# Optimization experiments

Measured on AMD Instinct MI355X. Metric: run time of the kernel, lower is better.

The kernel has to match this reference:

```python
import jax, jax.numpy as jnp
import numpy as np

BS, V, H, W = 2, 4, 24, 24
C, K, L, NH = 256, 16, 6, 8
DH = C // NH
FF = 4 * C
EPS = 1e-5


def _ln(x, w, b):
    m = jnp.mean(x, axis=-1, keepdims=True)
    v = jnp.mean((x - m) ** 2, axis=-1, keepdims=True)
    return (x - m) * jax.lax.rsqrt(v + EPS) * w + b


def _pe(x, W1, b1, W2, b2):
    # PositionEmbeddingLearnedMLP: Linear(3,C) -> ReLU -> Linear(C,C), channels-last
    return jax.nn.relu(x @ W1.T + b1) @ W2.T + b2


def setup_inputs():
    key = jax.random.key(0)
    ks = jax.random.split(key, 8)
    s = 0.02
    return {
        "feature": jax.random.normal(ks[0], (BS * V, C, H, W), jnp.float32),
        "xyz": jax.random.uniform(ks[1], (BS * V, H, W, 3), jnp.float32),
        "pe_W1": jax.random.normal(ks[2], (C, 3), jnp.float32) * s,
        "pe_b1": jnp.zeros((C,), jnp.float32),
        "pe_W2": jax.random.normal(ks[3], (C, C), jnp.float32) * s,
        "pe_b2": jnp.zeros((C,), jnp.float32),
        "Wqkv": jax.random.normal(ks[4], (L, 3 * C, C), jnp.float32) * s,
        "bqkv": jnp.zeros((L, 3 * C), jnp.float32),
        "Wo": jax.random.normal(ks[5], (L, C, C), jnp.float32) * s,
        "bo": jnp.zeros((L, C), jnp.float32),
        "ln_attn_w": jnp.ones((L, C), jnp.float32),
        "ln_attn_b": jnp.zeros((L, C), jnp.float32),
        "W1": jax.random.normal(ks[6], (L, FF, C), jnp.float32) * s,
        "b1": jnp.zeros((L, FF), jnp.float32),
        "W2": jax.random.normal(ks[7], (L, C, FF), jnp.float32) * s,
        "b2": jnp.zeros((L, C), jnp.float32),
        "ln_ffn_w": jnp.ones((L, C), jnp.float32),
        "ln_ffn_b": jnp.zeros((L, C), jnp.float32),
        "ln_out_w": jnp.ones((L, C), jnp.float32),
        "ln_out_b": jnp.zeros((L, C), jnp.float32),
    }


def _forward(feature, xyz, pe_W1, pe_b1, pe_W2, pe_b2, Wqkv, bqkv, Wo, bo,
             ln_attn_w, ln_attn_b, W1, b1, W2, b2, ln_ffn_w, ln_ffn_b,
             ln_out_w, ln_out_b):
    N = V * H * W
    # (B*V,C,H,W) -> (BS,N,C) ; (B*V,H,W,3) -> (BS,N,3) : flatten views+pixels
    feat = feature.reshape(BS, V, C, H, W).transpose(0, 1, 3, 4, 2).reshape(BS, N, C)
    pts = xyz.reshape(BS, N, 3)
    # per-batch KNN (self included), mirroring pointops.queryandgroup
    d2 = jnp.sum((pts[:, :, None, :] - pts[:, None, :, :]) ** 2, axis=-1)  # (BS,N,N)
    _, idx = jax.lax.top_k(-d2, K)  # (BS,N,K) nearest-neighbor indices
    grouped = jax.vmap(lambda p, i: p[i])(pts, idx)  # (BS,N,K,3)
    rel = grouped - pts[:, :, None, :]  # relative coords (use_xyz=True)
    q_pe = _pe(jnp.zeros((3,), feat.dtype), pe_W1, pe_b1, pe_W2, pe_b2)  # (C,)
    k_pe = _pe(rel, pe_W1, pe_b1, pe_W2, pe_b2).reshape(BS * N, K, C)
    idx_g = (idx + (jnp.arange(BS) * N)[:, None, None]).reshape(BS * N, K)
    out = feat.reshape(BS * N, C)
    for i in range(L):
        keyf = out[idx_g]  # (BN,K,C) per-layer neighbor gather
        # CrossAttentionLayer, pre-norm
        t2 = _ln(out, ln_attn_w[i], ln_attn_b[i])
        q = (t2 + q_pe) @ Wqkv[i, :C].T + bqkv[i, :C]
        k = (keyf + k_pe) @ Wqkv[i, C:2 * C].T + bqkv[i, C:2 * C]
        v = keyf @ Wqkv[i, 2 * C:].T + bqkv[i, 2 * C:]
        qh = q.reshape(-1, NH, DH)
        kh = k.reshape(-1, K, NH, DH)
        vh = v.reshape(-1, K, NH, DH)
        att = jax.nn.softmax(jnp.einsum('bhd,bkhd->bhk', qh, kh) * (DH ** -0.5), axis=-1)
        ao = jnp.einsum('bhk,bkhd->bhd', att, vh).reshape(-1, C) @ Wo[i].T + bo[i]
        out = out + ao
        # FFNLayer, pre-norm
        t2 = _ln(out, ln_ffn_w[i], ln_ffn_b[i])
        out = out + (jax.nn.relu(t2 @ W1[i].T + b1[i]) @ W2[i].T + b2[i])
        # extra per-layer LayerNorm
        out = _ln(out, ln_out_w[i], ln_out_b[i])
    return out.reshape(BS, V, H, W, C).transpose(0, 1, 4, 2, 3).reshape(BS * V, C, H, W)


def reference(feature, xyz, pe_W1, pe_b1, pe_W2, pe_b2, Wqkv, bqkv, Wo, bo,
              ln_attn_w, ln_attn_b, W1, b1, W2, b2, ln_ffn_w, ln_ffn_b,
              ln_out_w, ln_out_b):
    return _forward(feature, xyz, pe_W1, pe_b1, pe_W2, pe_b2, Wqkv, bqkv, Wo, bo,
                    ln_attn_w, ln_attn_b, W1, b1, W2, b2, ln_ffn_w, ln_ffn_b,
                    ln_out_w, ln_out_b)
```

## Files before the change

### kernel.cpp

```cpp
#include <hip/hip_runtime.h>
#include <math.h>

#define BS_ 2
#define V_ 4
#define H_ 24
#define W_ 24
#define N_ (V_*H_*W_)
#define BN_ (BS_*N_)
#define C_ 256
#define K_ 16
#define L_ 6
#define NH_ 8
#define DH_ 32
#define FF_ 1024

typedef __attribute__((ext_vector_type(4))) float f32x4;
typedef __attribute__((ext_vector_type(8))) short bf16x8;

__device__ inline unsigned short f2bf(float x) {
    unsigned u = __float_as_uint(x);
    unsigned r = u + 0x7fffu + ((u >> 16) & 1u);
    return (unsigned short)(r >> 16);
}
__device__ inline float bf2f(unsigned short h) {
    return __uint_as_float(((unsigned)h) << 16);
}

__global__ __launch_bounds__(256) void f2bf_kernel(const float* __restrict__ in,
                                                   unsigned short* __restrict__ out, int n) {
    int i = blockIdx.x*256 + threadIdx.x;
    if (i < n) out[i] = f2bf(in[i]);
}

__global__ __launch_bounds__(256) void reshape_in_kernel(const float* __restrict__ f,
                                                         float* __restrict__ outF,
                                                         unsigned short* __restrict__ outB) {
    int bn = blockIdx.x, c = threadIdx.x;
    int b = bn / N_, rem = bn % N_;
    int v = rem / (H_*W_), hw = rem % (H_*W_);
    float x = f[(((size_t)(b*V_ + v)*C_ + c)*(H_*W_)) + hw];
    outF[(size_t)bn*C_ + c] = x;
    outB[(size_t)bn*C_ + c] = f2bf(x);
}

__global__ __launch_bounds__(256) void reshape_out_kernel(const float* __restrict__ in,
                                                          float* __restrict__ o) {
    int bn = blockIdx.x, c = threadIdx.x;
    int b = bn / N_, rem = bn % N_;
    int v = rem / (H_*W_), hw = rem % (H_*W_);
    o[(((size_t)(b*V_ + v)*C_ + c)*(H_*W_)) + hw] = in[(size_t)bn*C_ + c];
}

__global__ __launch_bounds__(256) void knn_kernel(const float* __restrict__ pts,
                                                  int* __restrict__ idx) {
    int wid = threadIdx.x >> 6, lane = threadIdx.x & 63;
    int point = blockIdx.x*4 + wid;
    int b = point / N_;
    int il = point % N_;
    __shared__ float ps[N_*3];
    for (int l = threadIdx.x; l < N_*3; l += 256) ps[l] = pts[(size_t)b*N_*3 + l];
    __syncthreads();
    float qx = ps[il*3], qy = ps[il*3+1], qz = ps[il*3+2];
    unsigned long long key[36];
    #pragma unroll
    for (int s = 0; s < 36; ++s) {
        int j = lane + 64*s;
        float dx = qx - ps[j*3], dy = qy - ps[j*3+1], dz = qz - ps[j*3+2];
        float d2 = dx*dx + dy*dy + dz*dz;
        key[s] = ((unsigned long long)__float_as_uint(d2) << 32) | (unsigned)j;
    }
    for (int it = 0; it < K_; ++it) {
        unsigned long long best = key[0];
        #pragma unroll
        for (int s = 1; s < 36; ++s) best = key[s] < best ? key[s] : best;
        #pragma unroll
        for (int off = 32; off; off >>= 1) {
            unsigned long long o = __shfl_xor(best, off, 64);
            if (o < best) best = o;
        }
        int wj = (int)(best & 0xffffffffu);
        if (lane == 0) idx[point*K_ + it] = b*N_ + wj;
        if ((wj & 63) == lane) {
            int sw = wj >> 6;
            #pragma unroll
            for (int s = 0; s < 36; ++s) if (s == sw) key[s] = ~0ull;
        }
    }
}

__global__ __launch_bounds__(256) void qpe_kernel(const float* __restrict__ b1,
                                                  const float* __restrict__ W2,
                                                  const float* __restrict__ b2,
                                                  float* __restrict__ qpe) {
    __shared__ float h[C_];
    int tid = threadIdx.x;
    h[tid] = fmaxf(b1[tid], 0.f);
    __syncthreads();
    float acc = 0.f;
    for (int j = 0; j < C_; ++j) acc += h[j] * W2[(size_t)tid*C_ + j];
    qpe[tid] = acc + b2[tid];
}

__global__ __launch_bounds__(256) void pe_hidden_kernel(const float* __restrict__ pts,
                                                        const int* __restrict__ idx,
                                                        const float* __restrict__ W1,
                                                        const float* __restrict__ b1,
                                                        unsigned short* __restrict__ hidden) {
    int point = blockIdx.x;
    int c = threadIdx.x;
    __shared__ float rel[K_][3];
    if (threadIdx.x < K_*3) {
        int k = threadIdx.x / 3, ax = threadIdx.x % 3;
        int j = idx[point*K_ + k];
        rel[k][ax] = pts[(size_t)j*3 + ax] - pts[(size_t)point*3 + ax];
    }
    __syncthreads();
    float w0 = W1[c*3], w1 = W1[c*3+1], w2 = W1[c*3+2], bb = b1[c];
    #pragma unroll
    for (int k = 0; k < K_; ++k) {
        float v = rel[k][0]*w0 + rel[k][1]*w1 + rel[k][2]*w2 + bb;
        hidden[((size_t)point*K_ + k)*C_ + c] = f2bf(fmaxf(v, 0.f));
    }
}

template<int ACT, bool RES, int OMODE>
__global__ __launch_bounds__(256) void gemm_bf16(const unsigned short* __restrict__ A,
                                                 const unsigned short* __restrict__ W,
                                                 const float* __restrict__ bias,
                                                 const float* __restrict__ res,
                                                 float* __restrict__ outF,
                                                 unsigned short* __restrict__ outB,
                                                 int M, int P, int K) {
    const int BK = 32;
    __shared__ unsigned short As[64][BK+8];
    __shared__ unsigned short Ws[64][BK+8];
    int tid = threadIdx.x;
    int wave = tid >> 6, lane = tid & 63;
    int wr = wave >> 1, wc = wave & 1;
    int m0 = blockIdx.y * 64, n0 = blockIdx.x * 64;
    f32x4 acc[2][2];
    #pragma unroll
    for (int i = 0; i < 2; ++i)
        #pragma unroll
        for (int j = 0; j < 2; ++j) acc[i][j] = (f32x4){0.f, 0.f, 0.f, 0.f};

    int r = tid >> 2, ch = tid & 3;
    for (int k0 = 0; k0 < K; k0 += BK) {
        *(bf16x8*)&As[r][ch*8] = *(const bf16x8*)&A[(size_t)(m0 + r)*K + k0 + ch*8];
        *(bf16x8*)&Ws[r][ch*8] = *(const bf16x8*)&W[(size_t)(n0 + r)*K + k0 + ch*8];
        __syncthreads();
        int kf = (lane >> 4) * 8;
        bf16x8 af[2], wf[2];
        #pragma unroll
        for (int i = 0; i < 2; ++i) af[i] = *(const bf16x8*)&As[wr*32 + i*16 + (lane & 15)][kf];
        #pragma unroll
        for (int j = 0; j < 2; ++j) wf[j] = *(const bf16x8*)&Ws[wc*32 + j*16 + (lane & 15)][kf];
        #pragma unroll
        for (int i = 0; i < 2; ++i)
            #pragma unroll
            for (int j = 0; j < 2; ++j)
                acc[i][j] = __builtin_amdgcn_mfma_f32_16x16x32_bf16(af[i], wf[j], acc[i][j], 0, 0, 0);
        __syncthreads();
    }
    #pragma unroll
    for (int i = 0; i < 2; ++i) {
        #pragma unroll
        for (int j = 0; j < 2; ++j) {
            #pragma unroll
            for (int rg = 0; rg < 4; ++rg) {
                int m = m0 + wr*32 + i*16 + (lane >> 4)*4 + rg;
                int p = n0 + wc*32 + j*16 + (lane & 15);
                float v = acc[i][j][rg] + bias[p];
                if (ACT == 1) v = fmaxf(v, 0.f);
                if (RES) v += res[(size_t)m*P + p];
                if (OMODE != 2) outF[(size_t)m*P + p] = v;
                if (OMODE != 0) outB[(size_t)m*P + p] = f2bf(v);
            }
        }
    }
}

__global__ __launch_bounds__(256) void r_kernel(const unsigned short* __restrict__ q,
                                                const unsigned short* __restrict__ Wk,
                                                unsigned short* __restrict__ r) {
    int p0 = blockIdx.x * 16;
    int h = blockIdx.y;
    int tid = threadIdx.x;
    __shared__ float qs[16][DH_];
    for (int l = tid; l < 16*DH_; l += 256) {
        int p = l >> 5, d = l & 31;
        qs[p][d] = bf2f(q[(size_t)(p0 + p)*C_ + h*DH_ + d]);
    }
    __syncthreads();
    float acc[16] = {};
    for (int d = 0; d < DH_; ++d) {
        float w = bf2f(Wk[(size_t)(h*DH_ + d)*C_ + tid]);
        #pragma unroll
        for (int p = 0; p < 16; ++p) acc[p] += qs[p][d] * w;
    }
    #pragma unroll
    for (int p = 0; p < 16; ++p)
        r[(size_t)(p0 + p)*(NH_*C_) + h*C_ + tid] = f2bf(acc[p]);
}

__global__ __launch_bounds__(256) void attn_kernel(const unsigned short* __restrict__ q,
                                                   const unsigned short* __restrict__ kv,
                                                   const unsigned short* __restrict__ kpe,
                                                   const unsigned short* __restrict__ r,
                                                   const int* __restrict__ idx,
                                                   unsigned short* __restrict__ ao) {
    int wid = threadIdx.x >> 6, lane = threadIdx.x & 63;
    int point = blockIdx.x*4 + wid;
    __shared__ __align__(16) unsigned short vs[4][K_][264];
    __shared__ __align__(16) float atts[4][NH_][K_];
    int row = lane & 15;
    int off8 = (lane >> 4) * 8;
    int idx_l = idx[point*K_ + row];

    #pragma unroll
    for (int t = 0; t < 8; ++t) {
        int vr = 2*t + (lane >> 5);
        int j = __shfl(idx_l, vr, 64);
        int cc = (lane & 31) * 8;
        *(bf16x8*)&vs[wid][vr][cc] = *(const bf16x8*)&kv[(size_t)j*512 + 256 + cc];
    }

    f32x4 acc = {0.f, 0.f, 0.f, 0.f};
    const bf16x8 zero8 = {0,0,0,0,0,0,0,0};
    #pragma unroll
    for (int s = 0; s < 8; ++s) {
        bf16x8 a = *(const bf16x8*)&kpe[((size_t)point*K_ + row)*C_ + s*32 + off8];
        bf16x8 b = zero8;
        if (row < 8) b = *(const bf16x8*)&r[(size_t)point*NH_*C_ + row*C_ + s*32 + off8];
        acc = __builtin_amdgcn_mfma_f32_16x16x32_bf16(a, b, acc, 0, 0, 0);
    }
    #pragma unroll
    for (int s = 0; s < 8; ++s) {
        bf16x8 a = *(const bf16x8*)&kv[(size_t)idx_l*512 + s*32 + off8];
        bf16x8 b = zero8;
        if (row == 8 + s) b = *(const bf16x8*)&q[(size_t)point*C_ + s*32 + off8];
        acc = __builtin_amdgcn_mfma_f32_16x16x32_bf16(a, b, acc, 0, 0, 0);
    }

    const float scale = 0.1767766952966369f;
    float sv[4], m = -1e30f;
    #pragma unroll
    for (int rg = 0; rg < 4; ++rg) {
        float o = __shfl_xor(acc[rg], 8, 64);
        sv[rg] = (acc[rg] + o) * scale;
        m = fmaxf(m, sv[rg]);
    }
    m = fmaxf(m, __shfl_xor(m, 16, 64));
    m = fmaxf(m, __shfl_xor(m, 32, 64));
    float sum = 0.f;
    #pragma unroll
    for (int rg = 0; rg < 4; ++rg) { sv[rg] = __expf(sv[rg] - m); sum += sv[rg]; }
    sum += __shfl_xor(sum, 16, 64);
    sum += __shfl_xor(sum, 32, 64);
    float inv = 1.f / sum;
    if (row < 8) {
        f32x4 av = { sv[0]*inv, sv[1]*inv, sv[2]*inv, sv[3]*inv };
        *(f32x4*)&atts[wid][row][(lane >> 4) * 4] = av;
    }

    int h = lane >> 3;
    float att_f[16];
    #pragma unroll
    for (int u = 0; u < 4; ++u) {
        f32x4 t4 = *(const f32x4*)&atts[wid][h][u*4];
        att_f[u*4+0] = t4[0]; att_f[u*4+1] = t4[1]; att_f[u*4+2] = t4[2]; att_f[u*4+3] = t4[3];
    }
    int cbase = lane * 4;
    float o0 = 0.f, o1 = 0.f, o2 = 0.f, o3 = 0.f;
    #pragma unroll
    for (int k = 0; k < K_; ++k) {
        unsigned long long vv = *(const unsigned long long*)&vs[wid][k][cbase];
        unsigned lo = (unsigned)vv, hi = (unsigned)(vv >> 32);
        float a = att_f[k];
        o0 += a * __uint_as_float(lo << 16);
        o1 += a * __uint_as_float(lo & 0xffff0000u);
        o2 += a * __uint_as_float(hi << 16);
        o3 += a * __uint_as_float(hi & 0xffff0000u);
    }
    unsigned p0 = (unsigned)f2bf(o0) | ((unsigned)f2bf(o1) << 16);
    unsigned p1 = (unsigned)f2bf(o2) | ((unsigned)f2bf(o3) << 16);
    unsigned out2[2] = { p0, p1 };
    *(unsigned long long*)&ao[(size_t)point*C_ + cbase] = *(const unsigned long long*)out2;
}

template<int OMODE>
__global__ __launch_bounds__(256) void ln_kernel(const float* __restrict__ in,
                                                 const float* __restrict__ w,
                                                 const float* __restrict__ b,
                                                 const float* __restrict__ addvec,
                                                 float* __restrict__ outF,
                                                 unsigned short* __restrict__ outB) {
    int row = blockIdx.x, tid = threadIdx.x;
    float x = in[(size_t)row*C_ + tid];
    __shared__ float red[4];
    float v = x;
    #pragma unroll
    for (int off = 32; off; off >>= 1) v += __shfl_xor(v, off, 64);
    if ((tid & 63) == 0) red[tid >> 6] = v;
    __syncthreads();
    float mean = (red[0]+red[1]+red[2]+red[3]) * (1.f/C_);
    __syncthreads();
    float dx = x - mean;
    v = dx*dx;
    #pragma unroll
    for (int off = 32; off; off >>= 1) v += __shfl_xor(v, off, 64);
    if ((tid & 63) == 0) red[tid >> 6] = v;
    __syncthreads();
    float var = (red[0]+red[1]+red[2]+red[3]) * (1.f/C_);
    float y = dx * rsqrtf(var + 1e-5f) * w[tid] + b[tid];
    if (addvec) y += addvec[tid];
    if (OMODE != 2) outF[(size_t)row*C_ + tid] = y;
    outB[(size_t)row*C_ + tid] = f2bf(y);
}

__global__ __launch_bounds__(256) void ln2_kernel(const float* __restrict__ in,
                                                  const float* __restrict__ w1, const float* __restrict__ b1v,
                                                  const float* __restrict__ w2, const float* __restrict__ b2v,
                                                  const float* __restrict__ qpe,
                                                  float* __restrict__ outF, unsigned short* __restrict__ outB,
                                                  unsigned short* __restrict__ outT2) {
    int row = blockIdx.x, tid = threadIdx.x;
    float x = in[(size_t)row*C_ + tid];
    __shared__ float red[4];
    float v = x;
    #pragma unroll
    for (int off = 32; off; off >>= 1) v += __shfl_xor(v, off, 64);
    if ((tid & 63) == 0) red[tid >> 6] = v;
    __syncthreads();
    float mean = (red[0]+red[1]+red[2]+red[3]) * (1.f/C_);
    __syncthreads();
    float dx = x - mean;
    v = dx*dx;
    #pragma unroll
    for (int off = 32; off; off >>= 1) v += __shfl_xor(v, off, 64);
    if ((tid & 63) == 0) red[tid >> 6] = v;
    __syncthreads();
    float var = (red[0]+red[1]+red[2]+red[3]) * (1.f/C_);
    float y = dx * rsqrtf(var + 1e-5f) * w1[tid] + b1v[tid];
    outF[(size_t)row*C_ + tid] = y;
    outB[(size_t)row*C_ + tid] = f2bf(y);
    v = y;
    #pragma unroll
    for (int off = 32; off; off >>= 1) v += __shfl_xor(v, off, 64);
    __syncthreads();
    if ((tid & 63) == 0) red[tid >> 6] = v;
    __syncthreads();
    float mean2 = (red[0]+red[1]+red[2]+red[3]) * (1.f/C_);
    __syncthreads();
    float dy = y - mean2;
    v = dy*dy;
    #pragma unroll
    for (int off = 32; off; off >>= 1) v += __shfl_xor(v, off, 64);
    if ((tid & 63) == 0) red[tid >> 6] = v;
    __syncthreads();
    float var2 = (red[0]+red[1]+red[2]+red[3]) * (1.f/C_);
    float z = dy * rsqrtf(var2 + 1e-5f) * w2[tid] + b2v[tid] + qpe[tid];
    outT2[(size_t)row*C_ + tid] = f2bf(z);
}

extern "C" void kernel_launch(void* const* d_in, const int* in_sizes, int n_in,
                              void* d_out, int out_size, void* d_ws, size_t ws_size,
                              hipStream_t stream) {
    const float* feature  = (const float*)d_in[0];
    const float* xyz      = (const float*)d_in[1];
    const float* pe_W1    = (const float*)d_in[2];
    const float* pe_b1    = (const float*)d_in[3];
    const float* pe_W2    = (const float*)d_in[4];
    const float* pe_b2    = (const float*)d_in[5];
    const float* Wqkv     = (const float*)d_in[6];
    const float* bqkv     = (const float*)d_in[7];
    const float* Wo       = (const float*)d_in[8];
    const float* bo       = (const float*)d_in[9];
    const float* ln_attn_w= (const float*)d_in[10];
    const float* ln_attn_b= (const float*)d_in[11];
    const float* W1       = (const float*)d_in[12];
    const float* b1       = (const float*)d_in[13];
    const float* W2       = (const float*)d_in[14];
    const float* b2       = (const float*)d_in[15];
    const float* ln_ffn_w = (const float*)d_in[16];
    const float* ln_ffn_b = (const float*)d_in[17];
    const float* ln_out_w = (const float*)d_in[18];
    const float* ln_out_b = (const float*)d_in[19];

    float* ws = (float*)d_ws;
    float* w_out = ws;
    float* w_qpe = w_out + (size_t)BN_*C_;
    unsigned short* bptr = (unsigned short*)(w_qpe + C_ + 64);
    unsigned short* b_out = bptr;  bptr += (size_t)BN_*C_;
    unsigned short* b_t2  = bptr;  bptr += (size_t)BN_*C_;
    unsigned short* b_q   = bptr;  bptr += (size_t)BN_*C_;
    unsigned short* b_kv  = bptr;  bptr += (size_t)BN_*512;
    unsigned short* b_ao  = bptr;  bptr += (size_t)BN_*C_;
    unsigned short* b_ffh = bptr;  bptr += (size_t)BN_*FF_;
    unsigned short* w_kpe = bptr;  bptr += (size_t)BN_*K_*C_;
    unsigned short* w_r   = bptr;  bptr += (size_t)BN_*NH_*C_;
    unsigned short* b_hid = bptr;  bptr += (size_t)BN_*K_*C_;
    unsigned short* bWpe  = bptr;  bptr += (size_t)C_*C_;
    unsigned short* bWqkv = bptr;  bptr += (size_t)L_*3*C_*C_;
    unsigned short* bWo   = bptr;  bptr += (size_t)L_*C_*C_;
    unsigned short* bW1   = bptr;  bptr += (size_t)L_*FF_*C_;
    unsigned short* bW2   = bptr;  bptr += (size_t)L_*C_*FF_;
    int* w_idx = (int*)bptr;

    f2bf_kernel<<<(C_*C_+255)/256, 256, 0, stream>>>(pe_W2, bWpe, C_*C_);
    f2bf_kernel<<<(L_*3*C_*C_+255)/256, 256, 0, stream>>>(Wqkv, bWqkv, L_*3*C_*C_);
    f2bf_kernel<<<(L_*C_*C_+255)/256, 256, 0, stream>>>(Wo, bWo, L_*C_*C_);
    f2bf_kernel<<<(L_*FF_*C_+255)/256, 256, 0, stream>>>(W1, bW1, L_*FF_*C_);
    f2bf_kernel<<<(L_*C_*FF_+255)/256, 256, 0, stream>>>(W2, bW2, L_*C_*FF_);

    reshape_in_kernel<<<BN_, 256, 0, stream>>>(feature, w_out, b_out);
    knn_kernel<<<BN_/4, 256, 0, stream>>>(xyz, w_idx);
    qpe_kernel<<<1, 256, 0, stream>>>(pe_b1, pe_W2, pe_b2, w_qpe);
    pe_hidden_kernel<<<BN_, 256, 0, stream>>>(xyz, w_idx, pe_W1, pe_b1, b_hid);
    gemm_bf16<0,false,2><<<dim3(C_/64, (BN_*K_)/64), 256, 0, stream>>>(
        b_hid, bWpe, pe_b2, nullptr, nullptr, w_kpe, BN_*K_, C_, C_);

    ln_kernel<2><<<BN_, 256, 0, stream>>>(w_out, ln_attn_w, ln_attn_b, w_qpe, nullptr, b_t2);

    for (int i = 0; i < L_; ++i) {
        const unsigned short* Wq = bWqkv + (size_t)i*3*C_*C_;
        const unsigned short* Wk = Wq + (size_t)C_*C_;
        const float* bq = bqkv + (size_t)i*3*C_;
        const float* bk = bq + C_;

        gemm_bf16<0,false,2><<<dim3(C_/64, BN_/64), 256, 0, stream>>>(
            b_t2, Wq, bq, nullptr, nullptr, b_q, BN_, C_, C_);
        gemm_bf16<0,false,2><<<dim3(512/64, BN_/64), 256, 0, stream>>>(
            b_out, Wk, bk, nullptr, nullptr, b_kv, BN_, 512, C_);
        r_kernel<<<dim3(BN_/16, NH_), 256, 0, stream>>>(b_q, Wk, w_r);
        attn_kernel<<<BN_/4, 256, 0, stream>>>(b_q, b_kv, w_kpe, w_r, w_idx, b_ao);
        gemm_bf16<0,true,0><<<dim3(C_/64, BN_/64), 256, 0, stream>>>(
            b_ao, bWo + (size_t)i*C_*C_, bo + i*C_, w_out, w_out, nullptr, BN_, C_, C_);

        ln_kernel<2><<<BN_, 256, 0, stream>>>(w_out, ln_ffn_w + i*C_, ln_ffn_b + i*C_, nullptr, nullptr, b_t2);
        gemm_bf16<1,false,2><<<dim3(FF_/64, BN_/64), 256, 0, stream>>>(
            b_t2, bW1 + (size_t)i*FF_*C_, b1 + i*FF_, nullptr, nullptr, b_ffh, BN_, FF_, C_);
        gemm_bf16<0,true,0><<<dim3(C_/64, BN_/64), 256, 0, stream>>>(
            b_ffh, bW2 + (size_t)i*C_*FF_, b2 + i*C_, w_out, w_out, nullptr, BN_, C_, FF_);

        if (i < L_-1) {
            ln2_kernel<<<BN_, 256, 0, stream>>>(w_out, ln_out_w + i*C_, ln_out_b + i*C_,
                                                ln_attn_w + (i+1)*C_, ln_attn_b + (i+1)*C_,
                                                w_qpe, w_out, b_out, b_t2);
        } else {
            ln_kernel<1><<<BN_, 256, 0, stream>>>(w_out, ln_out_w + i*C_, ln_out_b + i*C_, nullptr, w_out, b_out);
        }
    }

    reshape_out_kernel<<<BN_, 256, 0, stream>>>(w_out, (float*)d_out);
}
```

Baseline: 736.6 us.

## Fuse weight casts and QKV GEMMs, double-buffer GEMM, MFMA for r projection

The five weight fp32->bf16 conversion launches become one kernel that indexes into a contiguous destination. The Q and KV projection GEMMs are merged into a single launch, and the scalar r_kernel (q·Wk per head) is replaced by an MFMA-based kernel that loads a transposed Wk tile into LDS. The GEMM body now double-buffers LDS and prefetches the next K-tile into registers while the MFMAs run. KNN top-k min-reduction is split into four independent chains to raise ILP. Together these cut launch overhead and per-layer latency, at the cost of more LDS use and more complex indexing, and the merged conversion relies on the bf16 weight buffers being laid out contiguously.

Result: no change. 726.9 us (-1.3%).

```diff
diff --git a/kernel.cpp b/kernel.cpp
--- a/kernel.cpp
+++ b/kernel.cpp
@@ -26,10 +26,22 @@
     return __uint_as_float(((unsigned)h) << 16);
 }
 
-__global__ __launch_bounds__(256) void f2bf_kernel(const float* __restrict__ in,
-                                                   unsigned short* __restrict__ out, int n) {
+__global__ __launch_bounds__(256) void f2bf5_kernel(const float* __restrict__ s0,
+                                                    const float* __restrict__ s1,
+                                                    const float* __restrict__ s2,
+                                                    const float* __restrict__ s3,
+                                                    const float* __restrict__ s4,
+                                                    unsigned short* __restrict__ dst) {
+    const int c0 = 65536, c1 = 1245184, c2 = 1638400, c3 = 3211264, c4 = 4784128;
     int i = blockIdx.x*256 + threadIdx.x;
-    if (i < n) out[i] = f2bf(in[i]);
+    if (i >= c4) return;
+    float v;
+    if (i < c0)      v = s0[i];
+    else if (i < c1) v = s1[i - c0];
+    else if (i < c2) v = s2[i - c1];
+    else if (i < c3) v = s3[i - c2];
+    else             v = s4[i - c3];
+    dst[i] = f2bf(v);
 }
 
 __global__ __launch_bounds__(256) void reshape_in_kernel(const float* __restrict__ f,
@@ -70,9 +82,17 @@
         key[s] = ((unsigned long long)__float_as_uint(d2) << 32) | (unsigned)j;
     }
     for (int it = 0; it < K_; ++it) {
-        unsigned long long best = key[0];
-        #pragma unroll
-        for (int s = 1; s < 36; ++s) best = key[s] < best ? key[s] : best;
+        unsigned long long b0 = key[0], b1 = key[1], b2 = key[2], b3 = key[3];
+        #pragma unroll
+        for (int s = 4; s < 36; s += 4) {
+            b0 = key[s]   < b0 ? key[s]   : b0;
+            b1 = key[s+1] < b1 ? key[s+1] : b1;
+            b2 = key[s+2] < b2 ? key[s+2] : b2;
+            b3 = key[s+3] < b3 ? key[s+3] : b3;
+        }
+        unsigned long long m01 = b0 < b1 ? b0 : b1;
+        unsigned long long m23 = b2 < b3 ? b2 : b3;
+        unsigned long long best = m01 < m23 ? m01 : m23;
         #pragma unroll
         for (int off = 32; off; off >>= 1) {
             unsigned long long o = __shfl_xor(best, off, 64);
@@ -124,20 +144,18 @@
 }
 
 template<int ACT, bool RES, int OMODE>
-__global__ __launch_bounds__(256) void gemm_bf16(const unsigned short* __restrict__ A,
-                                                 const unsigned short* __restrict__ W,
-                                                 const float* __restrict__ bias,
-                                                 const float* __restrict__ res,
-                                                 float* __restrict__ outF,
-                                                 unsigned short* __restrict__ outB,
-                                                 int M, int P, int K) {
-    const int BK = 32;
-    __shared__ unsigned short As[64][BK+8];
-    __shared__ unsigned short Ws[64][BK+8];
+__device__ __forceinline__ void gemm_body(const unsigned short* __restrict__ A, int sA,
+                                          const unsigned short* __restrict__ W, int sW,
+                                          const float* __restrict__ bias, int bcol0,
+                                          const float* __restrict__ res,
+                                          float* __restrict__ outF,
+                                          unsigned short* __restrict__ outB,
+                                          int sO, int on0, int m0, int K) {
+    __shared__ unsigned short As[2][64][40];
+    __shared__ unsigned short Ws[2][64][40];
     int tid = threadIdx.x;
     int wave = tid >> 6, lane = tid & 63;
     int wr = wave >> 1, wc = wave & 1;
-    int m0 = blockIdx.y * 64, n0 = blockIdx.x * 64;
     f32x4 acc[2][2];
     #pragma unroll
     for (int i = 0; i < 2; ++i)
@@ -145,21 +163,35 @@
         for (int j = 0; j < 2; ++j) acc[i][j] = (f32x4){0.f, 0.f, 0.f, 0.f};
 
     int r = tid >> 2, ch = tid & 3;
-    for (int k0 = 0; k0 < K; k0 += BK) {
-        *(bf16x8*)&As[r][ch*8] = *(const bf16x8*)&A[(size_t)(m0 + r)*K + k0 + ch*8];
-        *(bf16x8*)&Ws[r][ch*8] = *(const bf16x8*)&W[(size_t)(n0 + r)*K + k0 + ch*8];
-        __syncthreads();
+    const unsigned short* pA = A + (size_t)(m0 + r)*sA + ch*8;
+    const unsigned short* pW = W + (size_t)r*sW + ch*8;
+    *(bf16x8*)&As[0][r][ch*8] = *(const bf16x8*)pA;
+    *(bf16x8*)&Ws[0][r][ch*8] = *(const bf16x8*)pW;
+    __syncthreads();
+    int nk = K >> 5;
+    for (int t = 0; t < nk; ++t) {
+        int cur = t & 1;
+        bool has_next = (t + 1 < nk);
+        bf16x8 la, lw;
+        if (has_next) {
+            la = *(const bf16x8*)(pA + (t+1)*32);
+            lw = *(const bf16x8*)(pW + (t+1)*32);
+        }
         int kf = (lane >> 4) * 8;
         bf16x8 af[2], wf[2];
         #pragma unroll
-        for (int i = 0; i < 2; ++i) af[i] = *(const bf16x8*)&As[wr*32 + i*16 + (lane & 15)][kf];
-        #pragma unroll
-        for (int j = 0; j < 2; ++j) wf[j] = *(const bf16x8*)&Ws[wc*32 + j*16 + (lane & 15)][kf];
+        for (int i = 0; i < 2; ++i) af[i] = *(const bf16x8*)&As[cur][wr*32 + i*16 + (lane & 15)][kf];
+        #pragma unroll
+        for (int j = 0; j < 2; ++j) wf[j] = *(const bf16x8*)&Ws[cur][wc*32 + j*16 + (lane & 15)][kf];
         #pragma unroll
         for (int i = 0; i < 2; ++i)
             #pragma unroll
             for (int j = 0; j < 2; ++j)
                 acc[i][j] = __builtin_amdgcn_mfma_f32_16x16x32_bf16(af[i], wf[j], acc[i][j], 0, 0, 0);
+        if (has_next) {
+            *(bf16x8*)&As[cur^1][r][ch*8] = la;
+            *(bf16x8*)&Ws[cur^1][r][ch*8] = lw;
+        }
         __syncthreads();
     }
     #pragma unroll
@@ -169,38 +201,89 @@
             #pragma unroll
             for (int rg = 0; rg < 4; ++rg) {
                 int m = m0 + wr*32 + i*16 + (lane >> 4)*4 + rg;
-                int p = n0 + wc*32 + j*16 + (lane & 15);
-                float v = acc[i][j][rg] + bias[p];
+                int pl = wc*32 + j*16 + (lane & 15);
+                float v = acc[i][j][rg];
+                if (bias) v += bias[bcol0 + pl];
                 if (ACT == 1) v = fmaxf(v, 0.f);
-                if (RES) v += res[(size_t)m*P + p];
-                if (OMODE != 2) outF[(size_t)m*P + p] = v;
-                if (OMODE != 0) outB[(size_t)m*P + p] = f2bf(v);
+                if (RES) v += res[(size_t)m*sO + on0 + pl];
+                if (OMODE != 2) outF[(size_t)m*sO + on0 + pl] = v;
+                if (OMODE != 0) outB[(size_t)m*sO + on0 + pl] = f2bf(v);
             }
         }
     }
 }
 
-__global__ __launch_bounds__(256) void r_kernel(const unsigned short* __restrict__ q,
-                                                const unsigned short* __restrict__ Wk,
-                                                unsigned short* __restrict__ r) {
-    int p0 = blockIdx.x * 16;
-    int h = blockIdx.y;
+template<int ACT, bool RES, int OMODE>
+__global__ __launch_bounds__(256) void gemm_k(const unsigned short* __restrict__ A,
+                                              const unsigned short* __restrict__ W,
+                                              const float* __restrict__ bias,
+                                              const float* __restrict__ res,
+                                              float* __restrict__ outF,
+                                              unsigned short* __restrict__ outB,
+                                              int P, int K) {
+    int n0 = blockIdx.x * 64, m0 = blockIdx.y * 64;
+    gemm_body<ACT,RES,OMODE>(A, K, W + (size_t)n0*K, K, bias, n0, res, outF, outB, P, n0, m0, K);
+}
+
+__global__ __launch_bounds__(256) void qkv_kernel(const unsigned short* __restrict__ t2,
+                                                  const unsigned short* __restrict__ outb,
+                                                  const unsigned short* __restrict__ Wqkv_l,
+                                                  const float* __restrict__ bqkv_l,
+                                                  unsigned short* __restrict__ b_q,
+                                                  unsigned short* __restrict__ b_kv) {
+    int bx = blockIdx.x;
+    int n0 = bx * 64;
+    int m0 = blockIdx.y * 64;
+    if (bx < 4) {
+        gemm_body<0,false,2>(t2, C_, Wqkv_l + (size_t)n0*C_, C_, bqkv_l, n0,
+                             nullptr, nullptr, b_q, 256, n0, m0, C_);
+    } else {
+        gemm_body<0,false,2>(outb, C_, Wqkv_l + (size_t)n0*C_, C_, bqkv_l, n0,
+                             nullptr, nullptr, b_kv, 512, n0 - 256, m0, C_);
+    }
+}
+
+__global__ __launch_bounds__(256) void rk_kernel(const unsigned short* __restrict__ q,
+                                                 const unsigned short* __restrict__ Wqkv_l,
+                                                 unsigned short* __restrict__ r) {
+    int n0 = blockIdx.x * 64, m0 = blockIdx.y * 64, h = blockIdx.z;
+    __shared__ unsigned short As[64][40];
+    __shared__ unsigned short Ws[64][40];
     int tid = threadIdx.x;
-    __shared__ float qs[16][DH_];
-    for (int l = tid; l < 16*DH_; l += 256) {
-        int p = l >> 5, d = l & 31;
-        qs[p][d] = bf2f(q[(size_t)(p0 + p)*C_ + h*DH_ + d]);
-    }
-    __syncthreads();
-    float acc[16] = {};
-    for (int d = 0; d < DH_; ++d) {
-        float w = bf2f(Wk[(size_t)(h*DH_ + d)*C_ + tid]);
-        #pragma unroll
-        for (int p = 0; p < 16; ++p) acc[p] += qs[p][d] * w;
-    }
-    #pragma unroll
-    for (int p = 0; p < 16; ++p)
-        r[(size_t)(p0 + p)*(NH_*C_) + h*C_ + tid] = f2bf(acc[p]);
+    int wave = tid >> 6, lane = tid & 63;
+    int wr = wave >> 1, wc = wave & 1;
+    *(bf16x8*)&As[tid>>2][(tid&3)*8] =
+        *(const bf16x8*)&q[(size_t)(m0 + (tid>>2))*C_ + h*DH_ + (tid&3)*8];
+    {
+        int d = tid >> 3, cg = tid & 7;
+        bf16x8 wv = *(const bf16x8*)&Wqkv_l[(size_t)(C_ + h*DH_ + d)*C_ + n0 + cg*8];
+        #pragma unroll
+        for (int j = 0; j < 8; ++j) Ws[cg*8 + j][d] = (unsigned short)wv[j];
+    }
+    __syncthreads();
+    int kf = (lane >> 4) * 8;
+    bf16x8 af[2], wf[2];
+    #pragma unroll
+    for (int i = 0; i < 2; ++i) af[i] = *(const bf16x8*)&As[wr*32 + i*16 + (lane & 15)][kf];
+    #pragma unroll
+    for (int j = 0; j < 2; ++j) wf[j] = *(const bf16x8*)&Ws[wc*32 + j*16 + (lane & 15)][kf];
+    f32x4 acc[2][2];
+    #pragma unroll
+    for (int i = 0; i < 2; ++i)
+        #pragma unroll
+        for (int j = 0; j < 2; ++j)
+            acc[i][j] = __builtin_amdgcn_mfma_f32_16x16x32_bf16(af[i], wf[j],
+                          (f32x4){0.f,0.f,0.f,0.f}, 0, 0, 0);
+    #pragma unroll
+    for (int i = 0; i < 2; ++i)
+        #pragma unroll
+        for (int j = 0; j < 2; ++j)
+            #pragma unroll
+            for (int rg = 0; rg < 4; ++rg) {
+                int m = m0 + wr*32 + i*16 + (lane >> 4)*4 + rg;
+                int pl = wc*32 + j*16 + (lane & 15);
+                r[(size_t)m*(NH_*C_) + h*C_ + n0 + pl] = f2bf(acc[i][j][rg]);
+            }
 }
 
 __global__ __launch_bounds__(256) void attn_kernel(const unsigned short* __restrict__ q,
@@ -407,41 +490,32 @@
     unsigned short* bW2   = bptr;  bptr += (size_t)L_*C_*FF_;
     int* w_idx = (int*)bptr;
 
-    f2bf_kernel<<<(C_*C_+255)/256, 256, 0, stream>>>(pe_W2, bWpe, C_*C_);
-    f2bf_kernel<<<(L_*3*C_*C_+255)/256, 256, 0, stream>>>(Wqkv, bWqkv, L_*3*C_*C_);
-    f2bf_kernel<<<(L_*C_*C_+255)/256, 256, 0, stream>>>(Wo, bWo, L_*C_*C_);
-    f2bf_kernel<<<(L_*FF_*C_+255)/256, 256, 0, stream>>>(W1, bW1, L_*FF_*C_);
-    f2bf_kernel<<<(L_*C_*FF_+255)/256, 256, 0, stream>>>(W2, bW2, L_*C_*FF_);
+    f2bf5_kernel<<<(4784128 + 255)/256, 256, 0, stream>>>(pe_W2, Wqkv, Wo, W1, W2, bWpe);
 
     reshape_in_kernel<<<BN_, 256, 0, stream>>>(feature, w_out, b_out);
     knn_kernel<<<BN_/4, 256, 0, stream>>>(xyz, w_idx);
     qpe_kernel<<<1, 256, 0, stream>>>(pe_b1, pe_W2, pe_b2, w_qpe);
     pe_hidden_kernel<<<BN_, 256, 0, stream>>>(xyz, w_idx, pe_W1, pe_b1, b_hid);
-    gemm_bf16<0,false,2><<<dim3(C_/64, (BN_*K_)/64), 256, 0, stream>>>(
-        b_hid, bWpe, pe_b2, nullptr, nullptr, w_kpe, BN_*K_, C_, C_);
+    gemm_k<0,false,2><<<dim3(C_/64, (BN_*K_)/64), 256, 0, stream>>>(
+        b_hid, bWpe, pe_b2, nullptr, nullptr, w_kpe, C_, C_);
 
     ln_kernel<2><<<BN_, 256, 0, stream>>>(w_out, ln_attn_w, ln_attn_b, w_qpe, nullptr, b_t2);
 
     for (int i = 0; i < L_; ++i) {
-        const unsigned short* Wq = bWqkv + (size_t)i*3*C_*C_;
-        const unsigned short* Wk = Wq + (size_t)C_*C_;
-        const float* bq = bqkv + (size_t)i*3*C_;
-        const float* bk = bq + C_;
-
-        gemm_bf16<0,false,2><<<dim3(C_/64, BN_/64), 256, 0, stream>>>(
-            b_t2, Wq, bq, nullptr, nullptr, b_q, BN_, C_, C_);
-        gemm_bf16<0,false,2><<<dim3(512/64, BN_/64), 256, 0, stream>>>(
-            b_out, Wk, bk, nullptr, nullptr, b_kv, BN_, 512, C_);
-        r_kernel<<<dim3(BN_/16, NH_), 256, 0, stream>>>(b_q, Wk, w_r);
+        const unsigned short* Wqkv_l = bWqkv + (size_t)i*3*C_*C_;
+        const float* bqkv_l = bqkv + (size_t)i*3*C_;
+
+        qkv_kernel<<<dim3(12, BN_/64), 256, 0, stream>>>(b_t2, b_out, Wqkv_l, bqkv_l, b_q, b_kv);
+        rk_kernel<<<dim3(4, BN_/64, NH_), 256, 0, stream>>>(b_q, Wqkv_l, w_r);
         attn_kernel<<<BN_/4, 256, 0, stream>>>(b_q, b_kv, w_kpe, w_r, w_idx, b_ao);
-        gemm_bf16<0,true,0><<<dim3(C_/64, BN_/64), 256, 0, stream>>>(
-            b_ao, bWo + (size_t)i*C_*C_, bo + i*C_, w_out, w_out, nullptr, BN_, C_, C_);
+        gemm_k<0,true,0><<<dim3(C_/64, BN_/64), 256, 0, stream>>>(
+            b_ao, bWo + (size_t)i*C_*C_, bo + i*C_, w_out, w_out, nullptr, C_, C_);
 
         ln_kernel<2><<<BN_, 256, 0, stream>>>(w_out, ln_ffn_w + i*C_, ln_ffn_b + i*C_, nullptr, nullptr, b_t2);
-        gemm_bf16<1,false,2><<<dim3(FF_/64, BN_/64), 256, 0, stream>>>(
-            b_t2, bW1 + (size_t)i*FF_*C_, b1 + i*FF_, nullptr, nullptr, b_ffh, BN_, FF_, C_);
-        gemm_bf16<0,true,0><<<dim3(C_/64, BN_/64), 256, 0, stream>>>(
-            b_ffh, bW2 + (size_t)i*C_*FF_, b2 + i*C_, w_out, w_out, nullptr, BN_, C_, FF_);
+        gemm_k<1,false,2><<<dim3(FF_/64, BN_/64), 256, 0, stream>>>(
+            b_t2, bW1 + (size_t)i*FF_*C_, b1 + i*FF_, nullptr, nullptr, b_ffh, FF_, C_);
+        gemm_k<0,true,0><<<dim3(C_/64, BN_/64), 256, 0, stream>>>(
+            b_ffh, bW2 + (size_t)i*C_*FF_, b2 + i*C_, w_out, w_out, nullptr, C_, FF_);
 
         if (i < L_-1) {
             ln2_kernel<<<BN_, 256, 0, stream>>>(w_out, ln_out_w + i*C_, ln_out_b + i*C_,
```
